# Kernel tuning notes

Measured on AMD Instinct MI355X. Metric: run time of the kernel, lower is better.

Reference implementation:

```python
import jax, jax.numpy as jnp
import numpy as np

B, S, C, H = 2, 4096, 1024, 8
D = C // H
KCONV = 7  # depthwise causal conv kernel size


def setup_inputs() -> dict:
    key = jax.random.key(0)
    k1, k2, k3, k4 = jax.random.split(key, 4)
    x = jax.random.normal(k1, (B, S, C), jnp.float32)
    Wqkv = jax.random.normal(k2, (C, 3 * C), jnp.float32) * (1.0 / np.sqrt(C))
    Wo = jax.random.normal(k3, (C, C), jnp.float32) * (1.0 / np.sqrt(C))
    conv_w = jax.random.normal(k4, (C, KCONV), jnp.float32) * (1.0 / np.sqrt(KCONV))
    return {"x": x, "Wqkv": Wqkv, "Wo": Wo, "conv_w": conv_w}


def _ripple(x, Wqkv, Wo, conv_w):
    b, s, c = x.shape
    d = c // H
    qkv = x @ Wqkv
    q, k, v = jnp.split(qkv, 3, axis=-1)

    def heads(t):
        return t.reshape(b, s, H, d).transpose(0, 2, 1, 3)  # [B,H,S,D]

    qh, kh, vh = heads(q), heads(k), heads(v)

    # --- branch 1: telescoping attention (offsets 0, 1, 2, 4, ..., 2^k) ---
    n_pow = int(np.floor(np.log2(s))) + 1
    offsets = jnp.concatenate([jnp.zeros((1,), jnp.int32),
                               (2 ** jnp.arange(n_pow)).astype(jnp.int32)])  # [K]
    pos = jnp.arange(s, dtype=jnp.int32)[:, None] - offsets[None, :]  # [S,K]
    valid = pos >= 0
    posc = jnp.clip(pos, 0)
    kg = kh[:, :, posc]  # [B,H,S,K,D] gathered keys
    vg = vh[:, :, posc]  # [B,H,S,K,D] gathered values
    sc = jnp.einsum('bhsd,bhskd->bhsk', qh, kg) / np.sqrt(d)
    sc = jnp.where(valid[None, None], sc, -jnp.inf)  # offset 0 always valid
    w = jax.nn.softmax(sc, axis=-1)
    tele = jnp.einsum('bhsk,bhskd->bhsd', w, vg)

    # --- branch 2: depthwise causal conv over value stream ---
    vpad = jnp.pad(v, ((0, 0), (KCONV - 1, 0), (0, 0)))  # left pad -> causal
    conv = jax.lax.conv_general_dilated(
        vpad.transpose(0, 2, 1),        # NCH
        conv_w[:, None, :],             # OIH, groups=C -> I=1
        window_strides=(1,), padding='VALID',
        feature_group_count=c,
        dimension_numbers=('NCH', 'OIH', 'NCH')).transpose(0, 2, 1)  # [B,S,C]
    conv_h = conv.reshape(b, s, H, d).transpose(0, 2, 1, 3)

    # --- branch 3: low-rank (linear) attention, elu+1 feature map ---
    fq = jax.nn.elu(qh) + 1.0
    fk = jax.nn.elu(kh) + 1.0
    kv = jnp.einsum('bhsd,bhse->bhde', fk, vh)        # [B,H,D,D]
    z = jnp.einsum('bhsd,bhd->bhs', fq, fk.sum(2))    # normalizer
    low = jnp.einsum('bhsd,bhde->bhse', fq, kv) / (z[..., None] + 1e-6)

    h = (tele + conv_h + low).transpose(0, 2, 1, 3).reshape(b, s, c)
    return h @ Wo


def reference(x, Wqkv, Wo, conv_w):
    # RippleAttentionBlock: h, _ = ripple_attn(x); return x + h
    return x + _ripple(x, Wqkv, Wo, conv_w)
```

## Files before the change

kernel.cpp:

```cpp
#include <hip/hip_runtime.h>
#include <hip/hip_bf16.h>

#define BATCH 2
#define SEQ   4096
#define CHN   1024
#define NH    8
#define HD    128
#define NQROWS (BATCH*SEQ)
#define QKVN  (3*CHN)
#define NOFF  14
#define KCONV 7
#define NCH   16
#define CHS   (SEQ/NCH)

typedef short bf16x8v __attribute__((ext_vector_type(8)));
typedef float f32x4v  __attribute__((ext_vector_type(4)));

__device__ __forceinline__ float b2f(short s) {
    return __uint_as_float(((unsigned)(unsigned short)s) << 16);
}
__device__ __forceinline__ unsigned short f2bu(float f) {
    __hip_bfloat16 h = __float2bfloat16(f);
    return *reinterpret_cast<unsigned short*>(&h);
}
__device__ __forceinline__ void gload16(const void* g, void* l) {
    __builtin_amdgcn_global_load_lds(
        (const __attribute__((address_space(1))) unsigned int*)g,
        (__attribute__((address_space(3))) unsigned int*)l, 16, 0, 0);
}

__global__ void k_cvt(const float* __restrict__ in, short* __restrict__ out, int n4) {
    int i = blockIdx.x * blockDim.x + threadIdx.x;
    int stride = gridDim.x * blockDim.x;
    for (; i < n4; i += stride) {
        float4 v = reinterpret_cast<const float4*>(in)[i];
        ushort4 o;
        o.x = f2bu(v.x); o.y = f2bu(v.y); o.z = f2bu(v.z); o.w = f2bu(v.w);
        reinterpret_cast<ushort4*>(out)[i] = o;
    }
}

__global__ void k_transpose_cvt(const float* __restrict__ in, short* __restrict__ out,
                                int R, int Cc) {
    __shared__ float tile[32][33];
    int bc = blockIdx.x * 32, br = blockIdx.y * 32;
    int tx = threadIdx.x & 31, ty = threadIdx.x >> 5;
    for (int i = 0; i < 32; i += 8)
        tile[ty + i][tx] = in[(size_t)(br + ty + i) * Cc + bc + tx];
    __syncthreads();
    for (int i = 0; i < 32; i += 8)
        out[(size_t)(bc + ty + i) * R + br + tx] = (short)f2bu(tile[tx][ty + i]);
}

template<int EPI>
__global__ __launch_bounds__(256)
void k_gemm_bt(const short* __restrict__ A, const short* __restrict__ Bt,
               short* __restrict__ Cb, float* __restrict__ Cf,
               const float* __restrict__ resid, int M, int N, int K) {
    __shared__ short As[128 * 32];
    __shared__ short Bs[128 * 32];
    int tid = threadIdx.x;
    int w = tid >> 6, lane = tid & 63;
    int nbn = N >> 7;
    int bm = blockIdx.x / nbn, bn = blockIdx.x % nbn;
    size_t m0 = (size_t)bm << 7, n0 = (size_t)bn << 7;
    int wr = (w >> 1) << 6, wc = (w & 1) << 6;
    int lr = lane & 15, lk = lane >> 4;
    f32x4v acc[4][4] = {};

    int f0 = w * 64 + lane, f1 = f0 + 256;
    int r0 = f0 >> 2, q0 = f0 & 3;
    int r1 = f1 >> 2, q1 = f1 & 3;
    const short* Ap0 = A + (m0 + r0) * K + q0 * 8;
    const short* Ap1 = A + (m0 + r1) * K + q1 * 8;
    const short* Bp0 = Bt + (n0 + r0) * K + q0 * 8;
    const short* Bp1 = Bt + (n0 + r1) * K + q1 * 8;
    short* Asl0 = As + (w * 64) * 8;
    short* Asl1 = As + (256 + w * 64) * 8;
    short* Bsl0 = Bs + (w * 64) * 8;
    short* Bsl1 = Bs + (256 + w * 64) * 8;

    for (int k0 = 0; k0 < K; k0 += 32) {
        gload16(Ap0 + k0, Asl0);
        gload16(Ap1 + k0, Asl1);
        gload16(Bp0 + k0, Bsl0);
        gload16(Bp1 + k0, Bsl1);
        __syncthreads();
        bf16x8v af[4], bfv[4];
        #pragma unroll
        for (int m = 0; m < 4; ++m)
            af[m] = *reinterpret_cast<const bf16x8v*>(As + (wr + m * 16 + lr) * 32 + lk * 8);
        #pragma unroll
        for (int n = 0; n < 4; ++n)
            bfv[n] = *reinterpret_cast<const bf16x8v*>(Bs + (wc + n * 16 + lr) * 32 + lk * 8);
        #pragma unroll
        for (int m = 0; m < 4; ++m)
            #pragma unroll
            for (int n = 0; n < 4; ++n)
                acc[m][n] = __builtin_amdgcn_mfma_f32_16x16x32_bf16(af[m], bfv[n], acc[m][n], 0, 0, 0);
        __syncthreads();
    }
    #pragma unroll
    for (int m = 0; m < 4; ++m) {
        size_t grow = m0 + wr + m * 16 + lk * 4;
        #pragma unroll
        for (int n = 0; n < 4; ++n) {
            size_t gcol = n0 + wc + n * 16 + lr;
            #pragma unroll
            for (int i = 0; i < 4; ++i) {
                size_t idx = (grow + i) * N + gcol;
                if (EPI == 0) Cb[idx] = (short)f2bu(acc[m][n][i]);
                else          Cf[idx] = resid[idx] + acc[m][n][i];
            }
        }
    }
}

__global__ __launch_bounds__(256)
void k_kvpart(const short* __restrict__ qkv, float* __restrict__ kvpart,
              float* __restrict__ kspart) {
    __shared__ float fk_lds[32 * 128];
    __shared__ short v_lds[32 * 128];
    int t = threadIdx.x;
    int w = t >> 6, lane = t & 63;
    int bid = blockIdx.x;
    int bh = bid / NCH, ch = bid % NCH;
    int b = bh >> 3, h = bh & 7;
    size_t rowbase = (size_t)b * SEQ + (size_t)ch * CHS;
    int d0 = (t >> 4) * 8, e0 = (t & 15) * 8;
    float kv[8][8] = {};
    float ks[8] = {};
    for (int sub = 0; sub < CHS / 32; ++sub) {
        #pragma unroll
        for (int j = 0; j < 2; ++j) {
            int f = j * 256 + t;
            int row = f >> 4, c0 = (f & 15) * 8;
            const short* kp = qkv + (rowbase + sub * 32 + row) * QKVN + CHN + h * HD + c0;
            bf16x8v k8 = *reinterpret_cast<const bf16x8v*>(kp);
            float* dst = fk_lds + row * 128 + c0;
            #pragma unroll
            for (int e = 0; e < 8; ++e) {
                float x = b2f(k8[e]);
                dst[e] = x > 0.f ? x + 1.f : __expf(x);
            }
        }
        #pragma unroll
        for (int j = 0; j < 2; ++j) {
            int f = j * 256 + w * 64 + lane;
            int row = f >> 4, c0 = (f & 15) * 8;
            gload16(qkv + (rowbase + sub * 32 + row) * QKVN + 2 * CHN + h * HD + c0,
                    v_lds + (j * 256 + w * 64) * 8);
        }
        __syncthreads();
        for (int ss = 0; ss < 32; ++ss) {
            float fa[8];
            *(float4*)&fa[0] = *(const float4*)&fk_lds[ss * 128 + d0];
            *(float4*)&fa[4] = *(const float4*)&fk_lds[ss * 128 + d0 + 4];
            bf16x8v vv = *reinterpret_cast<const bf16x8v*>(&v_lds[ss * 128 + e0]);
            float vb[8];
            #pragma unroll
            for (int e = 0; e < 8; ++e) vb[e] = b2f(vv[e]);
            #pragma unroll
            for (int i = 0; i < 8; ++i) {
                ks[i] += fa[i];
                #pragma unroll
                for (int e = 0; e < 8; ++e) kv[i][e] += fa[i] * vb[e];
            }
        }
        __syncthreads();
    }
    size_t obase = (size_t)bid * (128 * 128);
    #pragma unroll
    for (int i = 0; i < 8; ++i) {
        *(float4*)&kvpart[obase + (d0 + i) * 128 + e0]     = *(float4*)&kv[i][0];
        *(float4*)&kvpart[obase + (d0 + i) * 128 + e0 + 4] = *(float4*)&kv[i][4];
    }
    if ((t & 15) == 0)
        #pragma unroll
        for (int i = 0; i < 8; ++i)
            kspart[(size_t)bid * 128 + d0 + i] = ks[i];
}

__global__ void k_kvreduce(const float* __restrict__ kvpart, const float* __restrict__ kspart,
                           short* __restrict__ kvt, float* __restrict__ ksum) {
    int idx = blockIdx.x * blockDim.x + threadIdx.x;
    const int total_kv = 16 * 128 * 128;
    if (idx < total_kv) {
        int bh = idx >> 14;
        int r = idx & 16383;
        int d = r >> 7, e = r & 127;
        float s = 0.f;
        const float* p = kvpart + (size_t)bh * NCH * 16384 + r;
        #pragma unroll
        for (int c = 0; c < NCH; ++c) s += p[(size_t)c * 16384];
        kvt[((size_t)bh << 14) + e * 128 + d] = (short)f2bu(s);
    } else {
        int k = idx - total_kv;
        if (k < 16 * 128) {
            int bh = k >> 7, d = k & 127;
            float s = 0.f;
            const float* p = kspart + (size_t)bh * NCH * 128 + d;
            #pragma unroll
            for (int c = 0; c < NCH; ++c) s += p[c * 128];
            ksum[k] = s;
        }
    }
}

__global__ __launch_bounds__(256)
void k_middle(const short* __restrict__ qkv, const short* __restrict__ kvt,
              const float* __restrict__ ksum, const float* __restrict__ conv_w,
              short* __restrict__ hbuf) {
    __shared__ short kvt_lds[128 * 128];
    __shared__ short q_lds[32 * 128];
    __shared__ short fq_lds[32 * 128];
    __shared__ float low_lds[32 * 128];
    __shared__ float ksum_lds[128];
    __shared__ float cw_lds[128 * KCONV];
    int t = threadIdx.x;
    int w = t >> 6, lane = t & 63;
    int bid = blockIdx.x;
    int bh = bid >> 7, chunk = bid & 127;
    int b = bh >> 3, h = bh & 7;
    int s0 = chunk * 32;
    size_t rowbase = (size_t)b * SEQ;

    {
        const short* src = kvt + ((size_t)bh << 14);
        #pragma unroll
        for (int j = 0; j < 8; ++j) {
            int f = j * 256 + w * 64;
            gload16(src + (size_t)(f + lane) * 8, kvt_lds + (size_t)f * 8);
        }
    }
    {
        #pragma unroll
        for (int j = 0; j < 2; ++j) {
            int f = j * 256 + w * 64 + lane;
            int row = f >> 4, c0 = (f & 15) * 8;
            gload16(qkv + (rowbase + s0 + row) * QKVN + h * HD + c0,
                    q_lds + (size_t)(j * 256 + w * 64) * 8);
        }
    }
    if (t < 128) ksum_lds[t] = ksum[bh * 128 + t];
    for (int f = t; f < 128 * KCONV; f += 256) {
        int d = f / KCONV, j = f % KCONV;
        cw_lds[f] = conv_w[(h * HD + d) * KCONV + j];
    }
    __syncthreads();
    #pragma unroll
    for (int j = 0; j < 2; ++j) {
        int f = j * 256 + t;
        bf16x8v qv8 = *reinterpret_cast<const bf16x8v*>(q_lds + f * 8);
        bf16x8v fq8;
        #pragma unroll
        for (int e = 0; e < 8; ++e) {
            float x = b2f(qv8[e]);
            float fx = x > 0.f ? x + 1.f : __expf(x);
            fq8[e] = (short)f2bu(fx);
        }
        *reinterpret_cast<bf16x8v*>(fq_lds + f * 8) = fq8;
    }
    __syncthreads();
    {
        int lr = lane & 15, lk = lane >> 4;
        f32x4v lacc[2][2] = {};
        #pragma unroll
        for (int ksb = 0; ksb < 4; ++ksb) {
            bf16x8v af[2], bfv[2];
            #pragma unroll
            for (int m = 0; m < 2; ++m)
                af[m] = *reinterpret_cast<const bf16x8v*>(fq_lds + (m * 16 + lr) * 128 + ksb * 32 + lk * 8);
            #pragma unroll
            for (int n = 0; n < 2; ++n)
                bfv[n] = *reinterpret_cast<const bf16x8v*>(kvt_lds + (w * 32 + n * 16 + lr) * 128 + ksb * 32 + lk * 8);
            #pragma unroll
            for (int m = 0; m < 2; ++m)
                #pragma unroll
                for (int n = 0; n < 2; ++n)
                    lacc[m][n] = __builtin_amdgcn_mfma_f32_16x16x32_bf16(af[m], bfv[n], lacc[m][n], 0, 0, 0);
        }
        #pragma unroll
        for (int m = 0; m < 2; ++m)
            #pragma unroll
            for (int n = 0; n < 2; ++n)
                #pragma unroll
                for (int i = 0; i < 4; ++i)
                    low_lds[(m * 16 + lk * 4 + i) * 128 + w * 32 + n * 16 + lr] = lacc[m][n][i];
    }
    int row = t >> 3, j8 = t & 7;
    int e0 = j8 * 16;
    int sl = s0 + row;
    float zp = 0.f;
    #pragma unroll
    for (int d = 0; d < 16; ++d)
        zp += b2f(fq_lds[row * 128 + e0 + d]) * ksum_lds[e0 + d];
    zp += __shfl_xor(zp, 1); zp += __shfl_xor(zp, 2); zp += __shfl_xor(zp, 4);
    float z = zp + 1e-6f;
    float qv[16];
    #pragma unroll
    for (int d = 0; d < 16; ++d) qv[d] = b2f(q_lds[row * 128 + e0 + d]);
    float scb[NOFF];
    #pragma unroll
    for (int o = 0; o < NOFF; ++o) {
        int off = (o == 0) ? 0 : (1 << (o - 1));
        int p = sl - off;
        float acc = 0.f;
        if (p >= 0) {
            const short* kp = qkv + (rowbase + p) * QKVN + CHN + h * HD + e0;
            bf16x8v k0v = *(const bf16x8v*)kp;
            bf16x8v k1v = *(const bf16x8v*)(kp + 8);
            #pragma unroll
            for (int d = 0; d < 8; ++d) acc += qv[d] * b2f(k0v[d]);
            #pragma unroll
            for (int d = 0; d < 8; ++d) acc += qv[8 + d] * b2f(k1v[d]);
        }
        scb[o] = acc;
    }
    #pragma unroll
    for (int o = 0; o < NOFF; ++o) {
        float v = scb[o];
        v += __shfl_xor(v, 1); v += __shfl_xor(v, 2); v += __shfl_xor(v, 4);
        scb[o] = v * 0.08838834764831845f;
    }
    float mmax = -1e30f;
    #pragma unroll
    for (int o = 0; o < NOFF; ++o) {
        int off = (o == 0) ? 0 : (1 << (o - 1));
        if (sl - off >= 0 && scb[o] > mmax) mmax = scb[o];
    }
    float wsum = 0.f;
    float tacc[16] = {};
    #pragma unroll
    for (int o = 0; o < NOFF; ++o) {
        int off = (o == 0) ? 0 : (1 << (o - 1));
        int p = sl - off;
        if (p < 0) continue;
        float wv = __expf(scb[o] - mmax);
        wsum += wv;
        const short* vp = qkv + (rowbase + p) * QKVN + 2 * CHN + h * HD + e0;
        bf16x8v v0 = *(const bf16x8v*)vp;
        bf16x8v v1 = *(const bf16x8v*)(vp + 8);
        #pragma unroll
        for (int d = 0; d < 8; ++d) tacc[d]     += wv * b2f(v0[d]);
        #pragma unroll
        for (int d = 0; d < 8; ++d) tacc[8 + d] += wv * b2f(v1[d]);
    }
    float inv_wsum = 1.f / wsum;
    float cacc[16] = {};
    #pragma unroll
    for (int jj = 0; jj < KCONV; ++jj) {
        int p = sl - 6 + jj;
        if (p < 0) continue;
        const short* vp = qkv + (rowbase + p) * QKVN + 2 * CHN + h * HD + e0;
        bf16x8v v0 = *(const bf16x8v*)vp;
        bf16x8v v1 = *(const bf16x8v*)(vp + 8);
        #pragma unroll
        for (int d = 0; d < 8; ++d) cacc[d]     += b2f(v0[d]) * cw_lds[(e0 + d) * KCONV + jj];
        #pragma unroll
        for (int d = 0; d < 8; ++d) cacc[8 + d] += b2f(v1[d]) * cw_lds[(e0 + 8 + d) * KCONV + jj];
    }
    __syncthreads();
    short outv[16];
    #pragma unroll
    for (int d = 0; d < 16; ++d) {
        float hval = tacc[d] * inv_wsum + cacc[d] + low_lds[row * 128 + e0 + d] / z;
        outv[d] = (short)f2bu(hval);
    }
    bf16x8v* op = (bf16x8v*)(hbuf + (rowbase + sl) * CHN + h * HD + e0);
    op[0] = *(bf16x8v*)&outv[0];
    op[1] = *(bf16x8v*)&outv[8];
}

extern "C" void kernel_launch(void* const* d_in, const int* in_sizes, int n_in,
                              void* d_out, int out_size, void* d_ws, size_t ws_size,
                              hipStream_t stream) {
    const float* x      = (const float*)d_in[0];
    const float* Wqkv   = (const float*)d_in[1];
    const float* Wo     = (const float*)d_in[2];
    const float* conv_w = (const float*)d_in[3];
    float* out = (float*)d_out;

    char* ws = (char*)d_ws;
    size_t off = 0;
    auto alloc = [&](size_t bytes) {
        char* p = ws + off;
        off += (bytes + 255) & ~(size_t)255;
        return (void*)p;
    };
    short* xb     = (short*)alloc((size_t)NQROWS * CHN * 2);
    short* wqkvT  = (short*)alloc((size_t)QKVN * CHN * 2);
    short* woT    = (short*)alloc((size_t)CHN * CHN * 2);
    short* qkv    = (short*)alloc((size_t)NQROWS * QKVN * 2);
    short* hbuf   = (short*)alloc((size_t)NQROWS * CHN * 2);
    float* kvpart = (float*)alloc((size_t)16 * NCH * 128 * 128 * 4);
    float* kspart = (float*)alloc((size_t)16 * NCH * 128 * 4);
    short* kvt    = (short*)alloc((size_t)16 * 128 * 128 * 2);
    float* ksum   = (float*)alloc((size_t)16 * 128 * 4);

    k_cvt<<<2048, 256, 0, stream>>>(x, xb, NQROWS * CHN / 4);
    k_transpose_cvt<<<dim3(QKVN / 32, CHN / 32), 256, 0, stream>>>(Wqkv, wqkvT, CHN, QKVN);
    k_transpose_cvt<<<dim3(CHN / 32, CHN / 32), 256, 0, stream>>>(Wo, woT, CHN, CHN);
    k_gemm_bt<0><<<(NQROWS / 128) * (QKVN / 128), 256, 0, stream>>>(
        xb, wqkvT, qkv, nullptr, nullptr, NQROWS, QKVN, CHN);
    k_kvpart<<<16 * NCH, 256, 0, stream>>>(qkv, kvpart, kspart);
    k_kvreduce<<<(16 * 128 * 128 + 16 * 128) / 256, 256, 0, stream>>>(kvpart, kspart, kvt, ksum);
    k_middle<<<16 * 128, 256, 0, stream>>>(qkv, kvt, ksum, conv_w, hbuf);
    k_gemm_bt<1><<<(NQROWS / 128) * (CHN / 128), 256, 0, stream>>>(
        hbuf, woT, nullptr, out, x, NQROWS, CHN, CHN);
}
```

Before: 324.0 us.

## Split kv partial kernel over value halves and drop LDS staging in middle kernel

The kv-partial kernel now splits the value dimension into two halves, doubling its grid from 256 to 512 blocks and halving per-thread accumulators. The catch is that each key tile is loaded and transformed twice. The reduce kernel is re-indexed for the new partial layout. The middle kernel no longer stages kvt and q in shared memory and reads them straight from global, which cuts LDS use (for occupancy) and one barrier but relies on cache hits for the repeated reads.

```diff
diff --git a/kernel.cpp b/kernel.cpp
--- a/kernel.cpp
+++ b/kernel.cpp
@@ -14,6 +14,7 @@
 #define CHS   (SEQ/NCH)
 
 typedef short bf16x8v __attribute__((ext_vector_type(8)));
+typedef short bf16x4v __attribute__((ext_vector_type(4)));
 typedef float f32x4v  __attribute__((ext_vector_type(4)));
 
 __device__ __forceinline__ float b2f(short s) {
@@ -120,23 +121,28 @@
 void k_kvpart(const short* __restrict__ qkv, float* __restrict__ kvpart,
               float* __restrict__ kspart) {
     __shared__ float fk_lds[32 * 128];
-    __shared__ short v_lds[32 * 128];
+    __shared__ short v_lds[32 * 64];
     int t = threadIdx.x;
     int w = t >> 6, lane = t & 63;
     int bid = blockIdx.x;
-    int bh = bid / NCH, ch = bid % NCH;
+    int eh = bid & 1;
+    int ch = (bid >> 1) & (NCH - 1);
+    int bh = bid / (NCH * 2);
     int b = bh >> 3, h = bh & 7;
     size_t rowbase = (size_t)b * SEQ + (size_t)ch * CHS;
-    int d0 = (t >> 4) * 8, e0 = (t & 15) * 8;
-    float kv[8][8] = {};
+    const short* kbase = qkv + CHN + h * HD;
+    const short* vbase = qkv + 2 * CHN + h * HD + eh * 64;
+    int d0 = (t >> 4) * 8;
+    int e0l = (t & 15) * 4;
+    float kv[8][4] = {};
     float ks[8] = {};
     for (int sub = 0; sub < CHS / 32; ++sub) {
         #pragma unroll
         for (int j = 0; j < 2; ++j) {
             int f = j * 256 + t;
             int row = f >> 4, c0 = (f & 15) * 8;
-            const short* kp = qkv + (rowbase + sub * 32 + row) * QKVN + CHN + h * HD + c0;
-            bf16x8v k8 = *reinterpret_cast<const bf16x8v*>(kp);
+            bf16x8v k8 = *reinterpret_cast<const bf16x8v*>(
+                kbase + (rowbase + sub * 32 + row) * QKVN + c0);
             float* dst = fk_lds + row * 128 + c0;
             #pragma unroll
             for (int e = 0; e < 8; ++e) {
@@ -144,41 +150,37 @@
                 dst[e] = x > 0.f ? x + 1.f : __expf(x);
             }
         }
-        #pragma unroll
-        for (int j = 0; j < 2; ++j) {
-            int f = j * 256 + w * 64 + lane;
-            int row = f >> 4, c0 = (f & 15) * 8;
-            gload16(qkv + (rowbase + sub * 32 + row) * QKVN + 2 * CHN + h * HD + c0,
-                    v_lds + (j * 256 + w * 64) * 8);
+        {
+            int f = w * 64 + lane;
+            gload16(vbase + (rowbase + sub * 32 + (f >> 3)) * QKVN + (f & 7) * 8,
+                    v_lds + (size_t)(w * 64) * 8);
         }
         __syncthreads();
         for (int ss = 0; ss < 32; ++ss) {
             float fa[8];
             *(float4*)&fa[0] = *(const float4*)&fk_lds[ss * 128 + d0];
             *(float4*)&fa[4] = *(const float4*)&fk_lds[ss * 128 + d0 + 4];
-            bf16x8v vv = *reinterpret_cast<const bf16x8v*>(&v_lds[ss * 128 + e0]);
-            float vb[8];
-            #pragma unroll
-            for (int e = 0; e < 8; ++e) vb[e] = b2f(vv[e]);
+            bf16x4v vv = *reinterpret_cast<const bf16x4v*>(&v_lds[ss * 64 + e0l]);
+            float vb[4];
+            #pragma unroll
+            for (int e = 0; e < 4; ++e) vb[e] = b2f(vv[e]);
             #pragma unroll
             for (int i = 0; i < 8; ++i) {
                 ks[i] += fa[i];
                 #pragma unroll
-                for (int e = 0; e < 8; ++e) kv[i][e] += fa[i] * vb[e];
+                for (int e = 0; e < 4; ++e) kv[i][e] += fa[i] * vb[e];
             }
         }
         __syncthreads();
     }
-    size_t obase = (size_t)bid * (128 * 128);
-    #pragma unroll
-    for (int i = 0; i < 8; ++i) {
-        *(float4*)&kvpart[obase + (d0 + i) * 128 + e0]     = *(float4*)&kv[i][0];
-        *(float4*)&kvpart[obase + (d0 + i) * 128 + e0 + 4] = *(float4*)&kv[i][4];
-    }
-    if ((t & 15) == 0)
+    size_t obase = (size_t)bid * (128 * 64);
+    #pragma unroll
+    for (int i = 0; i < 8; ++i)
+        *(float4*)&kvpart[obase + (d0 + i) * 64 + e0l] = *(float4*)&kv[i][0];
+    if ((t & 15) == 0 && eh == 0)
         #pragma unroll
         for (int i = 0; i < 8; ++i)
-            kspart[(size_t)bid * 128 + d0 + i] = ks[i];
+            kspart[(size_t)(bh * NCH + ch) * 128 + d0 + i] = ks[i];
 }
 
 __global__ void k_kvreduce(const float* __restrict__ kvpart, const float* __restrict__ kspart,
@@ -189,10 +191,11 @@
         int bh = idx >> 14;
         int r = idx & 16383;
         int d = r >> 7, e = r & 127;
+        int ehalf = e >> 6, el = e & 63;
         float s = 0.f;
-        const float* p = kvpart + (size_t)bh * NCH * 16384 + r;
-        #pragma unroll
-        for (int c = 0; c < NCH; ++c) s += p[(size_t)c * 16384];
+        const float* p = kvpart + ((size_t)(bh * NCH) * 2 + ehalf) * 8192 + d * 64 + el;
+        #pragma unroll
+        for (int c = 0; c < NCH; ++c) s += p[(size_t)c * 2 * 8192];
         kvt[((size_t)bh << 14) + e * 128 + d] = (short)f2bu(s);
     } else {
         int k = idx - total_kv;
@@ -211,8 +214,6 @@
 void k_middle(const short* __restrict__ qkv, const short* __restrict__ kvt,
               const float* __restrict__ ksum, const float* __restrict__ conv_w,
               short* __restrict__ hbuf) {
-    __shared__ short kvt_lds[128 * 128];
-    __shared__ short q_lds[32 * 128];
     __shared__ short fq_lds[32 * 128];
     __shared__ float low_lds[32 * 128];
     __shared__ float ksum_lds[128];
@@ -224,46 +225,34 @@
     int b = bh >> 3, h = bh & 7;
     int s0 = chunk * 32;
     size_t rowbase = (size_t)b * SEQ;
-
-    {
-        const short* src = kvt + ((size_t)bh << 14);
-        #pragma unroll
-        for (int j = 0; j < 8; ++j) {
-            int f = j * 256 + w * 64;
-            gload16(src + (size_t)(f + lane) * 8, kvt_lds + (size_t)f * 8);
-        }
-    }
-    {
-        #pragma unroll
-        for (int j = 0; j < 2; ++j) {
-            int f = j * 256 + w * 64 + lane;
-            int row = f >> 4, c0 = (f & 15) * 8;
-            gload16(qkv + (rowbase + s0 + row) * QKVN + h * HD + c0,
-                    q_lds + (size_t)(j * 256 + w * 64) * 8);
-        }
-    }
+    const short* qbase = qkv + h * HD;
+    const short* kbase = qkv + CHN + h * HD;
+    const short* vbase = qkv + 2 * CHN + h * HD;
+
     if (t < 128) ksum_lds[t] = ksum[bh * 128 + t];
     for (int f = t; f < 128 * KCONV; f += 256) {
         int d = f / KCONV, j = f % KCONV;
         cw_lds[f] = conv_w[(h * HD + d) * KCONV + j];
     }
-    __syncthreads();
     #pragma unroll
     for (int j = 0; j < 2; ++j) {
         int f = j * 256 + t;
-        bf16x8v qv8 = *reinterpret_cast<const bf16x8v*>(q_lds + f * 8);
+        int row = f >> 4, c0 = (f & 15) * 8;
+        bf16x8v q8 = *reinterpret_cast<const bf16x8v*>(
+            qbase + (rowbase + s0 + row) * QKVN + c0);
         bf16x8v fq8;
         #pragma unroll
         for (int e = 0; e < 8; ++e) {
-            float x = b2f(qv8[e]);
+            float x = b2f(q8[e]);
             float fx = x > 0.f ? x + 1.f : __expf(x);
             fq8[e] = (short)f2bu(fx);
         }
-        *reinterpret_cast<bf16x8v*>(fq_lds + f * 8) = fq8;
+        *reinterpret_cast<bf16x8v*>(fq_lds + row * 128 + c0) = fq8;
     }
     __syncthreads();
     {
         int lr = lane & 15, lk = lane >> 4;
+        const short* kvg = kvt + ((size_t)bh << 14);
         f32x4v lacc[2][2] = {};
         #pragma unroll
         for (int ksb = 0; ksb < 4; ++ksb) {
@@ -273,7 +262,7 @@
                 af[m] = *reinterpret_cast<const bf16x8v*>(fq_lds + (m * 16 + lr) * 128 + ksb * 32 + lk * 8);
             #pragma unroll
             for (int n = 0; n < 2; ++n)
-                bfv[n] = *reinterpret_cast<const bf16x8v*>(kvt_lds + (w * 32 + n * 16 + lr) * 128 + ksb * 32 + lk * 8);
+                bfv[n] = *reinterpret_cast<const bf16x8v*>(kvg + (w * 32 + n * 16 + lr) * 128 + ksb * 32 + lk * 8);
             #pragma unroll
             for (int m = 0; m < 2; ++m)
                 #pragma unroll
@@ -298,8 +287,13 @@
     zp += __shfl_xor(zp, 1); zp += __shfl_xor(zp, 2); zp += __shfl_xor(zp, 4);
     float z = zp + 1e-6f;
     float qv[16];
-    #pragma unroll
-    for (int d = 0; d < 16; ++d) qv[d] = b2f(q_lds[row * 128 + e0 + d]);
+    {
+        const short* qp = qbase + (rowbase + sl) * QKVN + e0;
+        bf16x8v q0 = *(const bf16x8v*)qp;
+        bf16x8v q1 = *(const bf16x8v*)(qp + 8);
+        #pragma unroll
+        for (int d = 0; d < 8; ++d) { qv[d] = b2f(q0[d]); qv[8 + d] = b2f(q1[d]); }
+    }
     float scb[NOFF];
     #pragma unroll
     for (int o = 0; o < NOFF; ++o) {
@@ -307,7 +301,7 @@
         int p = sl - off;
         float acc = 0.f;
         if (p >= 0) {
-            const short* kp = qkv + (rowbase + p) * QKVN + CHN + h * HD + e0;
+            const short* kp = kbase + (rowbase + p) * QKVN + e0;
             bf16x8v k0v = *(const bf16x8v*)kp;
             bf16x8v k1v = *(const bf16x8v*)(kp + 8);
             #pragma unroll
@@ -338,7 +332,7 @@
         if (p < 0) continue;
         float wv = __expf(scb[o] - mmax);
         wsum += wv;
-        const short* vp = qkv + (rowbase + p) * QKVN + 2 * CHN + h * HD + e0;
+        const short* vp = vbase + (rowbase + p) * QKVN + e0;
         bf16x8v v0 = *(const bf16x8v*)vp;
         bf16x8v v1 = *(const bf16x8v*)(vp + 8);
         #pragma unroll
@@ -352,7 +346,7 @@
     for (int jj = 0; jj < KCONV; ++jj) {
         int p = sl - 6 + jj;
         if (p < 0) continue;
-        const short* vp = qkv + (rowbase + p) * QKVN + 2 * CHN + h * HD + e0;
+        const short* vp = vbase + (rowbase + p) * QKVN + e0;
         bf16x8v v0 = *(const bf16x8v*)vp;
         bf16x8v v1 = *(const bf16x8v*)(vp + 8);
         #pragma unroll
@@ -393,7 +387,7 @@
     short* woT    = (short*)alloc((size_t)CHN * CHN * 2);
     short* qkv    = (short*)alloc((size_t)NQROWS * QKVN * 2);
     short* hbuf   = (short*)alloc((size_t)NQROWS * CHN * 2);
-    float* kvpart = (float*)alloc((size_t)16 * NCH * 128 * 128 * 4);
+    float* kvpart = (float*)alloc((size_t)16 * NCH * 2 * 128 * 64 * 4);
     float* kspart = (float*)alloc((size_t)16 * NCH * 128 * 4);
     short* kvt    = (short*)alloc((size_t)16 * 128 * 128 * 2);
     float* ksum   = (float*)alloc((size_t)16 * 128 * 4);
@@ -403,7 +397,7 @@
     k_transpose_cvt<<<dim3(CHN / 32, CHN / 32), 256, 0, stream>>>(Wo, woT, CHN, CHN);
     k_gemm_bt<0><<<(NQROWS / 128) * (QKVN / 128), 256, 0, stream>>>(
         xb, wqkvT, qkv, nullptr, nullptr, NQROWS, QKVN, CHN);
-    k_kvpart<<<16 * NCH, 256, 0, stream>>>(qkv, kvpart, kspart);
+    k_kvpart<<<16 * NCH * 2, 256, 0, stream>>>(qkv, kvpart, kspart);
     k_kvreduce<<<(16 * 128 * 128 + 16 * 128) / 256, 256, 0, stream>>>(kvpart, kspart, kvt, ksum);
     k_middle<<<16 * 128, 256, 0, stream>>>(qkv, kvt, ksum, conv_w, hbuf);
     k_gemm_bt<1><<<(NQROWS / 128) * (CHN / 128), 256, 0, stream>>>(
```

Result: faster. 297.6 us (-8.1%).
